# Performance work log

Measured on AMD Instinct MI355X. Metric: run time of the kernel, lower is better.

The kernel has to match this reference:

```python
import jax, jax.numpy as jnp
import numpy as np

B = 4096; NA = 32; DIU = 128; DOU = 32; DIB = 256; DOB = 64; DH = 128; N = NA + 1


def setup_inputs() -> dict:
    key = jax.random.key(0)
    ks = jax.random.split(key, 40)
    kidx = [0]
    def rn(shape, scale=0.1):
        k = ks[kidx[0]]; kidx[0] += 1
        return jax.random.normal(k, shape, jnp.float32) * scale
    inp = {}
    inp['s'] = rn((B, DIU * NA + DIB), 1.0)
    inp['a'] = rn((B, DOU * NA + DOB), 1.0)
    for pre, din in (('ue', DIU + DOU), ('bs', DIB + DOB)):
        inp[pre + '_l1_w'] = rn((din, DH))
        inp[pre + '_l1_b'] = jnp.zeros((DH,), jnp.float32)
        inp[pre + '_l2_w'] = rn((DH, DH))
        inp[pre + '_l2_b'] = jnp.zeros((DH,), jnp.float32)
        for l in range(2):
            inp[pre + f'_gru_wih{l}'] = rn((3 * DH, DH))
            inp[pre + f'_gru_whh{l}'] = rn((3 * DH, DH))
            inp[pre + f'_gru_bih{l}'] = jnp.zeros((3 * DH,), jnp.float32)
            inp[pre + f'_gru_bhh{l}'] = jnp.zeros((3 * DH,), jnp.float32)
    inp['gat_w'] = rn((DH, DH))
    inp['gat_a'] = rn((2 * DH, 1))
    adj = np.zeros((N, N), np.float32)
    adj[1:, 0] = 1.0
    adj[0, 1:] = 1.0  # star graph, as in generate_adjacent_matrix
    inp['adj'] = jnp.asarray(adj)
    inp['ev1_w'] = rn((DH, DH))
    inp['ev1_b'] = jnp.zeros((DH,), jnp.float32)
    inp['ev2_w'] = rn((DH, 1))
    inp['ev2_b'] = jnp.zeros((1,), jnp.float32)
    return inp


def _gru_layer(x, wih, whh, bih, bhh):
    # x: [B, T, H]; torch GRU gate order (r, z, n), weights [3H, H]
    h0 = jnp.zeros((x.shape[0], whh.shape[1]), x.dtype)
    def step(h, xt):
        gi = xt @ wih.T + bih
        gh = h @ whh.T + bhh
        ir, iz, inn = jnp.split(gi, 3, axis=-1)
        hr, hz, hn = jnp.split(gh, 3, axis=-1)
        r = jax.nn.sigmoid(ir + hr)
        z = jax.nn.sigmoid(iz + hz)
        n = jnp.tanh(inn + r * hn)
        h_new = (1.0 - z) * n + z * h
        return h_new, h_new
    _, ys = jax.lax.scan(step, h0, jnp.swapaxes(x, 0, 1))
    return jnp.swapaxes(ys, 0, 1)


def _critic(si, ai, l1w, l1b, l2w, l2b, g0, g1):
    x = jax.nn.relu(jnp.concatenate([si, ai], axis=-1) @ l1w + l1b)
    x = jax.nn.sigmoid(x @ l2w + l2b)
    x = _gru_layer(x, *g0)
    x = _gru_layer(x, *g1)
    return x


def reference(s, a,
              ue_l1_w, ue_l1_b, ue_l2_w, ue_l2_b,
              ue_gru_wih0, ue_gru_whh0, ue_gru_bih0, ue_gru_bhh0,
              ue_gru_wih1, ue_gru_whh1, ue_gru_bih1, ue_gru_bhh1,
              bs_l1_w, bs_l1_b, bs_l2_w, bs_l2_b,
              bs_gru_wih0, bs_gru_whh0, bs_gru_bih0, bs_gru_bhh0,
              bs_gru_wih1, bs_gru_whh1, bs_gru_bih1, bs_gru_bhh1,
              gat_w, gat_a, adj, ev1_w, ev1_b, ev2_w, ev2_b):
    batch = s.shape[0]
    s_ue = s[:, :DIU * NA].reshape(batch, NA, DIU)
    s_bs = s[:, DIU * NA:].reshape(batch, 1, DIB)
    a_ue = a[:, :DOU * NA].reshape(batch, NA, DOU)
    a_bs = a[:, -DOB:].reshape(batch, 1, DOB)
    emb_ue = _critic(s_ue, a_ue, ue_l1_w, ue_l1_b, ue_l2_w, ue_l2_b,
                     (ue_gru_wih0, ue_gru_whh0, ue_gru_bih0, ue_gru_bhh0),
                     (ue_gru_wih1, ue_gru_whh1, ue_gru_bih1, ue_gru_bhh1))
    emb_bs = _critic(s_bs, a_bs, bs_l1_w, bs_l1_b, bs_l2_w, bs_l2_b,
                     (bs_gru_wih0, bs_gru_whh0, bs_gru_bih0, bs_gru_bhh0),
                     (bs_gru_wih1, bs_gru_whh1, bs_gru_bih1, bs_gru_bhh1))
    emb = jnp.concatenate([emb_ue, emb_bs], axis=1)  # [B, N, DH]
    # GAT layer
    Wh = emb @ gat_w                                  # [B, N, DH]
    Wh1 = Wh @ gat_a[:DH]                             # [B, N, 1]
    Wh2 = Wh @ gat_a[DH:]                             # [B, N, 1]
    e = jax.nn.leaky_relu(Wh1 + jnp.swapaxes(Wh2, 1, 2), negative_slope=0.01)
    att = jnp.where(adj > 0, e, jnp.float32(-9e15))
    att = jax.nn.softmax(att, axis=1)                 # NOTE: dim=1, as in source
    # dropout is identity in eval mode
    h_prime = jnp.einsum('bij,bjf->bf', att, Wh)      # matmul + sum over dim 1
    h_prime = jax.nn.elu(h_prime)
    x = jax.nn.relu(h_prime @ ev1_w + ev1_b)
    return x @ ev2_w + ev2_b                          # [B, 1]
```

## Files before the change

kernel.cpp:

```cpp
#include <hip/hip_runtime.h>


typedef unsigned short u16;
typedef __bf16  bf16x8  __attribute__((ext_vector_type(8)));
typedef short   short8  __attribute__((ext_vector_type(8)));
typedef u16     u16x4   __attribute__((ext_vector_type(4)));
typedef float   floatx4 __attribute__((ext_vector_type(4)));

#define DEVI __device__ __forceinline__
#define MFMA(a, b, c) __builtin_amdgcn_mfma_f32_16x16x32_bf16((a), (b), (c), 0, 0, 0)

DEVI u16 f2b(float f) {
    unsigned u = __float_as_uint(f);
    u += 0x7fffu + ((u >> 16) & 1u);
    return (u16)(u >> 16);
}
DEVI float b2f(u16 s) { return __uint_as_float(((unsigned)s) << 16); }
DEVI float sigm(float x) { return 1.f / (1.f + __expf(-x)); }
DEVI float tanh_(float x) { return 1.f - 2.f / (__expf(2.f * x) + 1.f); }

DEVI bf16x8 ldfrag(const u16* q) {
    return *reinterpret_cast<const bf16x8*>(q);
}
DEVI bf16x8 ldfrag_f32(const float* q) {
    float4 u = *reinterpret_cast<const float4*>(q);
    float4 v = *reinterpret_cast<const float4*>(q + 4);
    short8 pk;
    pk[0] = (short)f2b(u.x); pk[1] = (short)f2b(u.y);
    pk[2] = (short)f2b(u.z); pk[3] = (short)f2b(u.w);
    pk[4] = (short)f2b(v.x); pk[5] = (short)f2b(v.y);
    pk[6] = (short)f2b(v.z); pk[7] = (short)f2b(v.w);
    return __builtin_bit_cast(bf16x8, pk);
}

enum : int {
    O_UE_W1T  = 0,
    O_UE_W2T  = 20480,
    O_UE_WIH0 = 36864,
    O_UE_WHH0 = 86016,
    O_UE_WIH1 = 135168,
    O_UE_WHH1 = 184320,
    O_BS_W1T  = 233472,
    O_BS_W2T  = 274432,
    O_BS_WIH0 = 290816,
    O_BS_WIH1 = 339968,
    O_GATWT   = 389120,
    O_EV1T    = 405504,
};
#define WB_X2   1048576u
#define WB_Y0   34603008u
#define WB_SSUM 139460608u

__global__ __launch_bounds__(256) void k_prep(
    const float* __restrict__ ue1, const float* __restrict__ ue2,
    const float* __restrict__ uw0, const float* __restrict__ uh0,
    const float* __restrict__ uw1, const float* __restrict__ uh1,
    const float* __restrict__ bs1, const float* __restrict__ bs2,
    const float* __restrict__ bw0, const float* __restrict__ bw1,
    const float* __restrict__ gw,  const float* __restrict__ e1,
    u16* __restrict__ out)
{
    const int tid = blockIdx.x * blockDim.x + threadIdx.x;
    const int stride = gridDim.x * blockDim.x;
    auto cvt = [&](const float* s, int off, int n) {
        for (int i = tid; i < n; i += stride) out[off + i] = f2b(s[i]);
    };
    auto tcv = [&](const float* s, int off, int K, int N) {
        const int tot = K * N;
        for (int i = tid; i < tot; i += stride) {
            int nn = i / K, kk = i - nn * K;
            out[off + i] = f2b(s[kk * N + nn]);
        }
    };
    tcv(ue1, O_UE_W1T, 160, 128);  tcv(ue2, O_UE_W2T, 128, 128);
    cvt(uw0, O_UE_WIH0, 49152);    cvt(uh0, O_UE_WHH0, 49152);
    cvt(uw1, O_UE_WIH1, 49152);    cvt(uh1, O_UE_WHH1, 49152);
    tcv(bs1, O_BS_W1T, 320, 128);  tcv(bs2, O_BS_W2T, 128, 128);
    cvt(bw0, O_BS_WIH0, 49152);    cvt(bw1, O_BS_WIH1, 49152);
    tcv(gw,  O_GATWT, 128, 128);   tcv(e1,  O_EV1T, 128, 128);
}

__global__ __launch_bounds__(512, 2) void k_ue_l1l2(
    const float* __restrict__ s, const float* __restrict__ a,
    const u16* __restrict__ W1T, const float* __restrict__ b1,
    const u16* __restrict__ W2T, const float* __restrict__ b2,
    u16* __restrict__ X2)
{
    __shared__ __align__(16) u16 A1[128][168];
    __shared__ __align__(16) u16 H[128][136];
    const int tid = threadIdx.x;
    const int w = tid >> 6, lane = tid & 63;
    const int lm = lane & 15, lg = lane >> 4;
    const int r0 = blockIdx.x * 128;

    bf16x8 bw1[5], bw2[4];
#pragma unroll
    for (int ks = 0; ks < 5; ++ks)
        bw1[ks] = ldfrag(W1T + (w * 16 + lm) * 160 + ks * 32 + lg * 8);
#pragma unroll
    for (int ks = 0; ks < 4; ++ks)
        bw2[ks] = ldfrag(W2T + (w * 16 + lm) * 128 + ks * 32 + lg * 8);
    const float bias1 = b1[w * 16 + lm];
    const float bias2 = b2[w * 16 + lm];

#pragma unroll
    for (int it = 0; it < 8; ++it) {
        const int fidx = it * 512 + tid;
        const int row = fidx >> 5, c4 = fidx & 31;
        const int r = r0 + row, bb = r >> 5, tt = r & 31;
        float4 v = *reinterpret_cast<const float4*>(s + (size_t)bb * 4352 + tt * 128 + c4 * 4);
        u16x4 p = {f2b(v.x), f2b(v.y), f2b(v.z), f2b(v.w)};
        *reinterpret_cast<u16x4*>(&A1[row][c4 * 4]) = p;
    }
#pragma unroll
    for (int it = 0; it < 2; ++it) {
        const int fidx = it * 512 + tid;
        const int row = fidx >> 3, c4 = fidx & 7;
        const int r = r0 + row, bb = r >> 5, tt = r & 31;
        float4 v = *reinterpret_cast<const float4*>(a + (size_t)bb * 1088 + tt * 32 + c4 * 4);
        u16x4 p = {f2b(v.x), f2b(v.y), f2b(v.z), f2b(v.w)};
        *reinterpret_cast<u16x4*>(&A1[row][128 + c4 * 4]) = p;
    }
    __syncthreads();

#pragma unroll
    for (int mt = 0; mt < 8; ++mt) {
        bf16x8 af[5];
#pragma unroll
        for (int ks = 0; ks < 5; ++ks)
            af[ks] = ldfrag(&A1[mt * 16 + lm][ks * 32 + lg * 8]);
        floatx4 acc = {0.f, 0.f, 0.f, 0.f};
#pragma unroll
        for (int ks = 0; ks < 5; ++ks) acc = MFMA(af[ks], bw1[ks], acc);
#pragma unroll
        for (int i = 0; i < 4; ++i) {
            float x = acc[i] + bias1;
            H[mt * 16 + lg * 4 + i][w * 16 + lm] = f2b(x > 0.f ? x : 0.f);
        }
    }
    __syncthreads();

#pragma unroll
    for (int mt = 0; mt < 8; ++mt) {
        bf16x8 af[4];
#pragma unroll
        for (int ks = 0; ks < 4; ++ks)
            af[ks] = ldfrag(&H[mt * 16 + lm][ks * 32 + lg * 8]);
        floatx4 acc = {0.f, 0.f, 0.f, 0.f};
#pragma unroll
        for (int ks = 0; ks < 4; ++ks) acc = MFMA(af[ks], bw2[ks], acc);
#pragma unroll
        for (int i = 0; i < 4; ++i)
            X2[(size_t)(r0 + mt * 16 + lg * 4 + i) * 128 + w * 16 + lm] =
                f2b(sigm(acc[i] + bias2));
    }
}

#define SCAN_STEP(RBUF, WBUF, XA, TCUR, PREF_T)                               \
  {                                                                           \
    bf16x8 af[4];                                                             \
    _Pragma("unroll") for (int ks = 0; ks < 4; ++ks)                          \
        af[ks] = ldfrag(&RBUF[lm][ks * 32 + lg * 8]);                         \
    floatx4 accR{0.f,0.f,0.f,0.f}, accZ{0.f,0.f,0.f,0.f};                     \
    floatx4 accGN{0.f,0.f,0.f,0.f}, accHN{0.f,0.f,0.f,0.f};                   \
    __builtin_amdgcn_s_setprio(1);                                            \
    _Pragma("unroll") for (int ks = 0; ks < 4; ++ks) {                        \
        accR  = MFMA(XA[ks], bwi[0][ks], accR);                               \
        accZ  = MFMA(XA[ks], bwi[1][ks], accZ);                               \
        accGN = MFMA(XA[ks], bwi[2][ks], accGN);                              \
    }                                                                         \
    if ((PREF_T) < 32) {                                                      \
        _Pragma("unroll") for (int ks = 0; ks < 4; ++ks)                      \
            XA[ks] = ldfrag(xp + (PREF_T) * 128 + ks * 32);                   \
    }                                                                         \
    _Pragma("unroll") for (int ks = 0; ks < 4; ++ks) {                        \
        accR = MFMA(af[ks], bwh[0][ks], accR);                                \
        accZ = MFMA(af[ks], bwh[1][ks], accZ);                                \
        accHN = MFMA(af[ks], bwh[2][ks], accHN);                              \
    }                                                                         \
    __builtin_amdgcn_s_setprio(0);                                            \
    _Pragma("unroll") for (int i = 0; i < 4; ++i) {                           \
        const float rr = sigm(accR[i] + br);                                  \
        const float zz = sigm(accZ[i] + bz);                                  \
        const float nn = tanh_(accGN[i] + bni + rr * (accHN[i] + bnh));       \
        const float hn = (1.f - zz) * nn + zz * hreg[i];                      \
        hreg[i] = hn;                                                         \
        if (MODE == 1) ssum[i] += hn;                                         \
        const u16 hv = f2b(hn);                                               \
        WBUF[lg * 4 + i][c] = hv;                                             \
        if (MODE == 0)                                                        \
            Y[((size_t)(b0 + lg * 4 + i) * 32 + (TCUR)) * 128 + c] = hv;      \
    }                                                                         \
    __builtin_amdgcn_sched_barrier(0);                                        \
    asm volatile("s_waitcnt lgkmcnt(0)" ::: "memory");                        \
    __builtin_amdgcn_s_barrier();                                             \
    __builtin_amdgcn_sched_barrier(0);                                        \
  }

template <int MODE>
__global__ __launch_bounds__(512, 2) void k_scan(
    const u16* __restrict__ X, const u16* __restrict__ WIH,
    const u16* __restrict__ WHH,
    const float* __restrict__ bih, const float* __restrict__ bhh,
    u16* __restrict__ Y, float* __restrict__ Ssum)
{
    __shared__ __align__(16) u16 hb0[16][136];
    __shared__ __align__(16) u16 hb1[16][136];
    const int w = threadIdx.x >> 6, lane = threadIdx.x & 63;
    const int lm = lane & 15, lg = lane >> 4;
    const int b0 = blockIdx.x * 16;
    const int c = w * 16 + lm;

    bf16x8 bwh[3][4], bwi[3][4];
#pragma unroll
    for (int g = 0; g < 3; ++g)
#pragma unroll
        for (int ks = 0; ks < 4; ++ks) {
            bwh[g][ks] = ldfrag(WHH + (g * 128 + c) * 128 + ks * 32 + lg * 8);
            bwi[g][ks] = ldfrag(WIH + (g * 128 + c) * 128 + ks * 32 + lg * 8);
        }

    for (int i = threadIdx.x; i < 16 * 136; i += 512) {
        ((u16*)hb0)[i] = 0; ((u16*)hb1)[i] = 0;
    }

    const float br  = bih[c] + bhh[c];
    const float bz  = bih[128 + c] + bhh[128 + c];
    const float bni = bih[256 + c], bnh = bhh[256 + c];

    const u16* xp = X + (size_t)(b0 + lm) * 32 * 128 + lg * 8;
    bf16x8 xa[4], xb[4];
#pragma unroll
    for (int ks = 0; ks < 4; ++ks) {
        xa[ks] = ldfrag(xp + ks * 32);
        xb[ks] = ldfrag(xp + 128 + ks * 32);
    }

    float hreg[4] = {}, ssum[4] = {};
    __syncthreads();

    for (int tt = 0; tt < 32; tt += 2) {
        SCAN_STEP(hb0, hb1, xa, tt,     tt + 2);
        SCAN_STEP(hb1, hb0, xb, tt + 1, tt + 3);
    }
    if (MODE == 1) {
#pragma unroll
        for (int i = 0; i < 4; ++i)
            Ssum[(size_t)(b0 + lg * 4 + i) * 128 + c] = ssum[i];
    }
}

__global__ __launch_bounds__(256, 2) void k_bs_final(
    const float* __restrict__ s, const float* __restrict__ a,
    const u16* __restrict__ W1T, const float* __restrict__ b1,
    const u16* __restrict__ W2T, const float* __restrict__ b2,
    const u16* __restrict__ WIH0, const float* __restrict__ bih0,
    const float* __restrict__ bhh0,
    const u16* __restrict__ WIH1, const float* __restrict__ bih1,
    const float* __restrict__ bhh1,
    const float* __restrict__ Ssum,
    const u16* __restrict__ GATWT, const u16* __restrict__ EV1T,
    const float* __restrict__ ev1b, const float* __restrict__ ev2w,
    const float* __restrict__ ev2b, float* __restrict__ out)
{
    __shared__ __align__(16) char smem[52224];
    u16   (*X2L)[136] = reinterpret_cast<u16(*)[136]>(smem);
    u16   (*HBP)[136] = reinterpret_cast<u16(*)[136]>(smem + 17408);
    u16   (*H0L)[136] = reinterpret_cast<u16(*)[136]>(smem + 34816);
    float (*HL)[132]  = reinterpret_cast<float(*)[132]>(smem);
    u16   (*HBF)[136] = reinterpret_cast<u16(*)[136]>(smem + 34816);
    float (*XBF)[132] = reinterpret_cast<float(*)[132]>(smem);

    const int w = threadIdx.x >> 6, lane = threadIdx.x & 63;
    const int lm = lane & 15, lg = lane >> 4;
    const int r0 = blockIdx.x * 64 + w * 16;
    const int lr = w * 16;

    {
        const float* srow = s + (size_t)(r0 + lm) * 4352 + 4096 + lg * 8;
        const float* arow = a + (size_t)(r0 + lm) * 1088 + 1024 + lg * 8;
        bf16x8 af[10];
#pragma unroll
        for (int ks = 0; ks < 8; ++ks) af[ks] = ldfrag_f32(srow + ks * 32);
        af[8] = ldfrag_f32(arow);
        af[9] = ldfrag_f32(arow + 32);

        const u16* wb1 = W1T + lm * 320 + lg * 8;
#pragma unroll
        for (int n = 0; n < 8; ++n) {
            floatx4 acc = {0.f, 0.f, 0.f, 0.f};
#pragma unroll
            for (int ks = 0; ks < 10; ++ks)
                acc = MFMA(af[ks], ldfrag(wb1 + n * 5120 + ks * 32), acc);
            const float bias = b1[n * 16 + lm];
#pragma unroll
            for (int i = 0; i < 4; ++i) {
                float x = acc[i] + bias;
                HBP[lr + lg * 4 + i][n * 16 + lm] = f2b(x > 0.f ? x : 0.f);
            }
        }
        __syncthreads();

        bf16x8 af2[4];
#pragma unroll
        for (int ks = 0; ks < 4; ++ks)
            af2[ks] = ldfrag(&HBP[lr + lm][ks * 32 + lg * 8]);
        const u16* wb2 = W2T + lm * 128 + lg * 8;
#pragma unroll
        for (int n = 0; n < 8; ++n) {
            floatx4 acc = {0.f, 0.f, 0.f, 0.f};
#pragma unroll
            for (int ks = 0; ks < 4; ++ks)
                acc = MFMA(af2[ks], ldfrag(wb2 + n * 2048 + ks * 32), acc);
            const float bias = b2[n * 16 + lm];
#pragma unroll
            for (int i = 0; i < 4; ++i)
                X2L[lr + lg * 4 + i][n * 16 + lm] = f2b(sigm(acc[i] + bias));
        }
    }
    __syncthreads();

    {
        bf16x8 ax[4];
#pragma unroll
        for (int ks = 0; ks < 4; ++ks)
            ax[ks] = ldfrag(&X2L[lr + lm][ks * 32 + lg * 8]);
        floatx4 acc[24];
#pragma unroll
        for (int j = 0; j < 24; ++j) acc[j] = floatx4{0.f, 0.f, 0.f, 0.f};
        const u16* wbp = WIH0 + lm * 128 + lg * 8;
#pragma unroll
        for (int j = 0; j < 24; ++j)
#pragma unroll
            for (int ks = 0; ks < 4; ++ks)
                acc[j] = MFMA(ax[ks], ldfrag(wbp + j * 2048 + ks * 32), acc[j]);
#pragma unroll
        for (int ct = 0; ct < 8; ++ct) {
            const int cc = ct * 16 + lm;
            const float brr = bih0[cc] + bhh0[cc];
            const float bzz = bih0[128 + cc] + bhh0[128 + cc];
            const float bni = bih0[256 + cc], bnh = bhh0[256 + cc];
#pragma unroll
            for (int i = 0; i < 4; ++i) {
                const float rr = sigm(acc[ct][i] + brr);
                const float zz = sigm(acc[8 + ct][i] + bzz);
                const float nn = tanh_(acc[16 + ct][i] + bni + rr * bnh);
                H0L[lr + lg * 4 + i][cc] = f2b((1.f - zz) * nn);
            }
        }
    }
    __syncthreads();

    {
        bf16x8 ax[4];
#pragma unroll
        for (int ks = 0; ks < 4; ++ks)
            ax[ks] = ldfrag(&H0L[lr + lm][ks * 32 + lg * 8]);
        floatx4 acc[24];
#pragma unroll
        for (int j = 0; j < 24; ++j) acc[j] = floatx4{0.f, 0.f, 0.f, 0.f};
        const u16* wbp = WIH1 + lm * 128 + lg * 8;
#pragma unroll
        for (int j = 0; j < 24; ++j)
#pragma unroll
            for (int ks = 0; ks < 4; ++ks)
                acc[j] = MFMA(ax[ks], ldfrag(wbp + j * 2048 + ks * 32), acc[j]);
        __syncthreads();
#pragma unroll
        for (int ct = 0; ct < 8; ++ct) {
            const int cc = ct * 16 + lm;
            const float brr = bih1[cc] + bhh1[cc];
            const float bzz = bih1[128 + cc] + bhh1[128 + cc];
            const float bni = bih1[256 + cc], bnh = bhh1[256 + cc];
#pragma unroll
            for (int i = 0; i < 4; ++i) {
                const float rr = sigm(acc[ct][i] + brr);
                const float zz = sigm(acc[8 + ct][i] + bzz);
                const float nn = tanh_(acc[16 + ct][i] + bni + rr * bnh);
                HL[lr + lg * 4 + i][cc] = (1.f - zz) * nn;
            }
        }
    }
    __syncthreads();

    {
        const float* p1 = Ssum + (size_t)(r0 + lm) * 128 + lg * 8;
        bf16x8 af[4];
#pragma unroll
        for (int ks = 0; ks < 4; ++ks) {
            float4 u  = *reinterpret_cast<const float4*>(p1 + ks * 32);
            float4 u2 = *reinterpret_cast<const float4*>(p1 + ks * 32 + 4);
            float4 v  = *reinterpret_cast<const float4*>(&HL[lr + lm][ks * 32 + lg * 8]);
            float4 v2 = *reinterpret_cast<const float4*>(&HL[lr + lm][ks * 32 + lg * 8 + 4]);
            short8 pk;
            pk[0] = (short)f2b(u.x + v.x);  pk[1] = (short)f2b(u.y + v.y);
            pk[2] = (short)f2b(u.z + v.z);  pk[3] = (short)f2b(u.w + v.w);
            pk[4] = (short)f2b(u2.x + v2.x); pk[5] = (short)f2b(u2.y + v2.y);
            pk[6] = (short)f2b(u2.z + v2.z); pk[7] = (short)f2b(u2.w + v2.w);
            af[ks] = __builtin_bit_cast(bf16x8, pk);
        }
        __syncthreads();
        const u16* gwp = GATWT + lm * 128 + lg * 8;
#pragma unroll
        for (int n = 0; n < 8; ++n) {
            floatx4 acc = {0.f, 0.f, 0.f, 0.f};
#pragma unroll
            for (int ks = 0; ks < 4; ++ks)
                acc = MFMA(af[ks], ldfrag(gwp + n * 2048 + ks * 32), acc);
#pragma unroll
            for (int i = 0; i < 4; ++i) {
                float x = acc[i];
                x = x > 0.f ? x : (__expf(x) - 1.f);
                HBF[lr + lg * 4 + i][n * 16 + lm] = f2b(x);
            }
        }
        __syncthreads();

        bf16x8 af2[4];
#pragma unroll
        for (int ks = 0; ks < 4; ++ks)
            af2[ks] = ldfrag(&HBF[lr + lm][ks * 32 + lg * 8]);
        const u16* e1p = EV1T + lm * 128 + lg * 8;
#pragma unroll
        for (int n = 0; n < 8; ++n) {
            floatx4 acc = {0.f, 0.f, 0.f, 0.f};
#pragma unroll
            for (int ks = 0; ks < 4; ++ks)
                acc = MFMA(af2[ks], ldfrag(e1p + n * 2048 + ks * 32), acc);
            const float bias = ev1b[n * 16 + lm];
#pragma unroll
            for (int i = 0; i < 4; ++i) {
                float v = acc[i] + bias;
                XBF[lr + lg * 4 + i][n * 16 + lm] = v > 0.f ? v : 0.f;
            }
        }
        __syncthreads();

        float sacc = 0.f;
#pragma unroll
        for (int k = 0; k < 32; ++k) {
            const int cc = lg * 32 + k;
            sacc += XBF[lr + lm][cc] * ev2w[cc];
        }
        sacc += __shfl_xor(sacc, 16, 64);
        sacc += __shfl_xor(sacc, 32, 64);
        if (lg == 0) out[r0 + lm] = sacc + ev2b[0];
    }
}

extern "C" void kernel_launch(void* const* d_in, const int* in_sizes, int n_in,
                              void* d_out, int out_size, void* d_ws, size_t ws_size,
                              hipStream_t stream)
{
    (void)in_sizes; (void)n_in; (void)out_size; (void)ws_size;
    const float* s       = (const float*)d_in[0];
    const float* a       = (const float*)d_in[1];
    const float* ue_l1_w = (const float*)d_in[2];
    const float* ue_l1_b = (const float*)d_in[3];
    const float* ue_l2_w = (const float*)d_in[4];
    const float* ue_l2_b = (const float*)d_in[5];
    const float* ue_wih0 = (const float*)d_in[6];
    const float* ue_whh0 = (const float*)d_in[7];
    const float* ue_bih0 = (const float*)d_in[8];
    const float* ue_bhh0 = (const float*)d_in[9];
    const float* ue_wih1 = (const float*)d_in[10];
    const float* ue_whh1 = (const float*)d_in[11];
    const float* ue_bih1 = (const float*)d_in[12];
    const float* ue_bhh1 = (const float*)d_in[13];
    const float* bs_l1_w = (const float*)d_in[14];
    const float* bs_l1_b = (const float*)d_in[15];
    const float* bs_l2_w = (const float*)d_in[16];
    const float* bs_l2_b = (const float*)d_in[17];
    const float* bs_wih0 = (const float*)d_in[18];
    const float* bs_bih0 = (const float*)d_in[20];
    const float* bs_bhh0 = (const float*)d_in[21];
    const float* bs_wih1 = (const float*)d_in[22];
    const float* bs_bih1 = (const float*)d_in[24];
    const float* bs_bhh1 = (const float*)d_in[25];
    const float* gat_w   = (const float*)d_in[26];
    const float* ev1_w   = (const float*)d_in[29];
    const float* ev1_b   = (const float*)d_in[30];
    const float* ev2_w   = (const float*)d_in[31];
    const float* ev2_b   = (const float*)d_in[32];

    char* ws = (char*)d_ws;
    u16*   wb   = (u16*)ws;
    u16*   X2   = (u16*)(ws + WB_X2);
    u16*   Y0   = (u16*)(ws + WB_Y0);
    float* SSUM = (float*)(ws + WB_SSUM);

    k_prep<<<256, 256, 0, stream>>>(ue_l1_w, ue_l2_w, ue_wih0, ue_whh0,
                                    ue_wih1, ue_whh1, bs_l1_w, bs_l2_w,
                                    bs_wih0, bs_wih1, gat_w, ev1_w, wb);
    k_ue_l1l2<<<1024, 512, 0, stream>>>(s, a, wb + O_UE_W1T, ue_l1_b,
                                        wb + O_UE_W2T, ue_l2_b, X2);
    k_scan<0><<<256, 512, 0, stream>>>(X2, wb + O_UE_WIH0, wb + O_UE_WHH0,
                                       ue_bih0, ue_bhh0, Y0, nullptr);
    k_scan<1><<<256, 512, 0, stream>>>(Y0, wb + O_UE_WIH1, wb + O_UE_WHH1,
                                       ue_bih1, ue_bhh1, nullptr, SSUM);
    k_bs_final<<<64, 256, 0, stream>>>(s, a, wb + O_BS_W1T, bs_l1_b,
                                       wb + O_BS_W2T, bs_l2_b,
                                       wb + O_BS_WIH0, bs_bih0, bs_bhh0,
                                       wb + O_BS_WIH1, bs_bih1, bs_bhh1,
                                       SSUM, wb + O_GATWT, wb + O_EV1T,
                                       ev1_b, ev2_w, ev2_b, (float*)d_out);
}
```

Before: 359.3 us.

## Repartition final BS kernel so each wave owns output columns, not rows

Restructures k_bs_final from 64 blocks of 4 waves, each wave computing all 128 output columns for its own 16 rows, to 256 blocks of 8 waves that share 16 rows, with each wave computing one 16-column slice. Every layer now exchanges activations through shared memory with a barrier between layers. The aim is to spread the BS critic tail across more CUs and cut per-wave serial MFMA chains and accumulator register pressure. The cost is more barriers and more weight-fragment loads per block, since each block rereads all weights for only 16 rows.

```diff
diff --git a/kernel.cpp b/kernel.cpp
--- a/kernel.cpp
+++ b/kernel.cpp
@@ -250,7 +250,7 @@
     }
 }
 
-__global__ __launch_bounds__(256, 2) void k_bs_final(
+__global__ __launch_bounds__(512, 1) void k_bs_final(
     const float* __restrict__ s, const float* __restrict__ a,
     const u16* __restrict__ W1T, const float* __restrict__ b1,
     const u16* __restrict__ W2T, const float* __restrict__ b2,
@@ -263,18 +263,17 @@
     const float* __restrict__ ev1b, const float* __restrict__ ev2w,
     const float* __restrict__ ev2b, float* __restrict__ out)
 {
-    __shared__ __align__(16) char smem[52224];
-    u16   (*X2L)[136] = reinterpret_cast<u16(*)[136]>(smem);
-    u16   (*HBP)[136] = reinterpret_cast<u16(*)[136]>(smem + 17408);
-    u16   (*H0L)[136] = reinterpret_cast<u16(*)[136]>(smem + 34816);
-    float (*HL)[132]  = reinterpret_cast<float(*)[132]>(smem);
-    u16   (*HBF)[136] = reinterpret_cast<u16(*)[136]>(smem + 34816);
-    float (*XBF)[132] = reinterpret_cast<float(*)[132]>(smem);
+    __shared__ __align__(16) u16 HBl[16][136];
+    __shared__ __align__(16) u16 X2b[16][136];
+    __shared__ __align__(16) u16 H0b[16][136];
+    __shared__ __align__(16) float HLf[16][132];
+    __shared__ __align__(16) u16 HBe[16][136];
+    __shared__ __align__(16) float XBf[16][132];
 
     const int w = threadIdx.x >> 6, lane = threadIdx.x & 63;
     const int lm = lane & 15, lg = lane >> 4;
-    const int r0 = blockIdx.x * 64 + w * 16;
-    const int lr = w * 16;
+    const int r0 = blockIdx.x * 16;
+    const int c = w * 16 + lm;
 
     {
         const float* srow = s + (size_t)(r0 + lm) * 4352 + 4096 + lg * 8;
@@ -285,166 +284,161 @@
         af[8] = ldfrag_f32(arow);
         af[9] = ldfrag_f32(arow + 32);
 
-        const u16* wb1 = W1T + lm * 320 + lg * 8;
-#pragma unroll
-        for (int n = 0; n < 8; ++n) {
-            floatx4 acc = {0.f, 0.f, 0.f, 0.f};
-#pragma unroll
-            for (int ks = 0; ks < 10; ++ks)
-                acc = MFMA(af[ks], ldfrag(wb1 + n * 5120 + ks * 32), acc);
-            const float bias = b1[n * 16 + lm];
-#pragma unroll
-            for (int i = 0; i < 4; ++i) {
-                float x = acc[i] + bias;
-                HBP[lr + lg * 4 + i][n * 16 + lm] = f2b(x > 0.f ? x : 0.f);
-            }
-        }
-        __syncthreads();
-
-        bf16x8 af2[4];
-#pragma unroll
-        for (int ks = 0; ks < 4; ++ks)
-            af2[ks] = ldfrag(&HBP[lr + lm][ks * 32 + lg * 8]);
-        const u16* wb2 = W2T + lm * 128 + lg * 8;
-#pragma unroll
-        for (int n = 0; n < 8; ++n) {
-            floatx4 acc = {0.f, 0.f, 0.f, 0.f};
-#pragma unroll
-            for (int ks = 0; ks < 4; ++ks)
-                acc = MFMA(af2[ks], ldfrag(wb2 + n * 2048 + ks * 32), acc);
-            const float bias = b2[n * 16 + lm];
-#pragma unroll
-            for (int i = 0; i < 4; ++i)
-                X2L[lr + lg * 4 + i][n * 16 + lm] = f2b(sigm(acc[i] + bias));
-        }
-    }
-    __syncthreads();
-
-    {
-        bf16x8 ax[4];
-#pragma unroll
-        for (int ks = 0; ks < 4; ++ks)
-            ax[ks] = ldfrag(&X2L[lr + lm][ks * 32 + lg * 8]);
-        floatx4 acc[24];
-#pragma unroll
-        for (int j = 0; j < 24; ++j) acc[j] = floatx4{0.f, 0.f, 0.f, 0.f};
-        const u16* wbp = WIH0 + lm * 128 + lg * 8;
-#pragma unroll
-        for (int j = 0; j < 24; ++j)
-#pragma unroll
-            for (int ks = 0; ks < 4; ++ks)
-                acc[j] = MFMA(ax[ks], ldfrag(wbp + j * 2048 + ks * 32), acc[j]);
-#pragma unroll
-        for (int ct = 0; ct < 8; ++ct) {
-            const int cc = ct * 16 + lm;
-            const float brr = bih0[cc] + bhh0[cc];
-            const float bzz = bih0[128 + cc] + bhh0[128 + cc];
-            const float bni = bih0[256 + cc], bnh = bhh0[256 + cc];
-#pragma unroll
-            for (int i = 0; i < 4; ++i) {
-                const float rr = sigm(acc[ct][i] + brr);
-                const float zz = sigm(acc[8 + ct][i] + bzz);
-                const float nn = tanh_(acc[16 + ct][i] + bni + rr * bnh);
-                H0L[lr + lg * 4 + i][cc] = f2b((1.f - zz) * nn);
-            }
-        }
-    }
-    __syncthreads();
-
-    {
-        bf16x8 ax[4];
-#pragma unroll
-        for (int ks = 0; ks < 4; ++ks)
-            ax[ks] = ldfrag(&H0L[lr + lm][ks * 32 + lg * 8]);
-        floatx4 acc[24];
-#pragma unroll
-        for (int j = 0; j < 24; ++j) acc[j] = floatx4{0.f, 0.f, 0.f, 0.f};
-        const u16* wbp = WIH1 + lm * 128 + lg * 8;
-#pragma unroll
-        for (int j = 0; j < 24; ++j)
-#pragma unroll
-            for (int ks = 0; ks < 4; ++ks)
-                acc[j] = MFMA(ax[ks], ldfrag(wbp + j * 2048 + ks * 32), acc[j]);
-        __syncthreads();
-#pragma unroll
-        for (int ct = 0; ct < 8; ++ct) {
-            const int cc = ct * 16 + lm;
-            const float brr = bih1[cc] + bhh1[cc];
-            const float bzz = bih1[128 + cc] + bhh1[128 + cc];
-            const float bni = bih1[256 + cc], bnh = bhh1[256 + cc];
-#pragma unroll
-            for (int i = 0; i < 4; ++i) {
-                const float rr = sigm(acc[ct][i] + brr);
-                const float zz = sigm(acc[8 + ct][i] + bzz);
-                const float nn = tanh_(acc[16 + ct][i] + bni + rr * bnh);
-                HL[lr + lg * 4 + i][cc] = (1.f - zz) * nn;
-            }
-        }
-    }
-    __syncthreads();
-
+        bf16x8 bw[10];
+#pragma unroll
+        for (int ks = 0; ks < 10; ++ks)
+            bw[ks] = ldfrag(W1T + c * 320 + ks * 32 + lg * 8);
+        floatx4 acc = {0.f, 0.f, 0.f, 0.f};
+#pragma unroll
+        for (int ks = 0; ks < 10; ++ks) acc = MFMA(af[ks], bw[ks], acc);
+        const float bias = b1[c];
+#pragma unroll
+        for (int i = 0; i < 4; ++i) {
+            float x = acc[i] + bias;
+            HBl[lg * 4 + i][c] = f2b(x > 0.f ? x : 0.f);
+        }
+    }
+    __syncthreads();
+
+    {
+        bf16x8 af[4], bw[4];
+#pragma unroll
+        for (int ks = 0; ks < 4; ++ks) {
+            af[ks] = ldfrag(&HBl[lm][ks * 32 + lg * 8]);
+            bw[ks] = ldfrag(W2T + c * 128 + ks * 32 + lg * 8);
+        }
+        floatx4 acc = {0.f, 0.f, 0.f, 0.f};
+#pragma unroll
+        for (int ks = 0; ks < 4; ++ks) acc = MFMA(af[ks], bw[ks], acc);
+        const float bias = b2[c];
+#pragma unroll
+        for (int i = 0; i < 4; ++i)
+            X2b[lg * 4 + i][c] = f2b(sigm(acc[i] + bias));
+    }
+    __syncthreads();
+
+    {
+        bf16x8 af[4], bw[3][4];
+#pragma unroll
+        for (int ks = 0; ks < 4; ++ks) {
+            af[ks] = ldfrag(&X2b[lm][ks * 32 + lg * 8]);
+#pragma unroll
+            for (int g = 0; g < 3; ++g)
+                bw[g][ks] = ldfrag(WIH0 + (g * 128 + c) * 128 + ks * 32 + lg * 8);
+        }
+        floatx4 aR{0,0,0,0}, aZ{0,0,0,0}, aN{0,0,0,0};
+#pragma unroll
+        for (int ks = 0; ks < 4; ++ks) {
+            aR = MFMA(af[ks], bw[0][ks], aR);
+            aZ = MFMA(af[ks], bw[1][ks], aZ);
+            aN = MFMA(af[ks], bw[2][ks], aN);
+        }
+        const float brr = bih0[c] + bhh0[c];
+        const float bzz = bih0[128 + c] + bhh0[128 + c];
+        const float bni = bih0[256 + c], bnh = bhh0[256 + c];
+#pragma unroll
+        for (int i = 0; i < 4; ++i) {
+            const float rr = sigm(aR[i] + brr);
+            const float zz = sigm(aZ[i] + bzz);
+            const float nn = tanh_(aN[i] + bni + rr * bnh);
+            H0b[lg * 4 + i][c] = f2b((1.f - zz) * nn);
+        }
+    }
+    __syncthreads();
+
+    float4 ssA[4], ssB[4];
     {
         const float* p1 = Ssum + (size_t)(r0 + lm) * 128 + lg * 8;
-        bf16x8 af[4];
-#pragma unroll
-        for (int ks = 0; ks < 4; ++ks) {
-            float4 u  = *reinterpret_cast<const float4*>(p1 + ks * 32);
-            float4 u2 = *reinterpret_cast<const float4*>(p1 + ks * 32 + 4);
-            float4 v  = *reinterpret_cast<const float4*>(&HL[lr + lm][ks * 32 + lg * 8]);
-            float4 v2 = *reinterpret_cast<const float4*>(&HL[lr + lm][ks * 32 + lg * 8 + 4]);
+#pragma unroll
+        for (int ks = 0; ks < 4; ++ks) {
+            ssA[ks] = *reinterpret_cast<const float4*>(p1 + ks * 32);
+            ssB[ks] = *reinterpret_cast<const float4*>(p1 + ks * 32 + 4);
+        }
+        bf16x8 af[4], bw[3][4];
+#pragma unroll
+        for (int ks = 0; ks < 4; ++ks) {
+            af[ks] = ldfrag(&H0b[lm][ks * 32 + lg * 8]);
+#pragma unroll
+            for (int g = 0; g < 3; ++g)
+                bw[g][ks] = ldfrag(WIH1 + (g * 128 + c) * 128 + ks * 32 + lg * 8);
+        }
+        floatx4 aR{0,0,0,0}, aZ{0,0,0,0}, aN{0,0,0,0};
+#pragma unroll
+        for (int ks = 0; ks < 4; ++ks) {
+            aR = MFMA(af[ks], bw[0][ks], aR);
+            aZ = MFMA(af[ks], bw[1][ks], aZ);
+            aN = MFMA(af[ks], bw[2][ks], aN);
+        }
+        const float brr = bih1[c] + bhh1[c];
+        const float bzz = bih1[128 + c] + bhh1[128 + c];
+        const float bni = bih1[256 + c], bnh = bhh1[256 + c];
+#pragma unroll
+        for (int i = 0; i < 4; ++i) {
+            const float rr = sigm(aR[i] + brr);
+            const float zz = sigm(aZ[i] + bzz);
+            const float nn = tanh_(aN[i] + bni + rr * bnh);
+            HLf[lg * 4 + i][c] = (1.f - zz) * nn;
+        }
+    }
+    __syncthreads();
+
+    {
+        bf16x8 af[4], bw[4];
+#pragma unroll
+        for (int ks = 0; ks < 4; ++ks) {
+            const float* hl = &HLf[lm][ks * 32 + lg * 8];
+            float4 v  = *reinterpret_cast<const float4*>(hl);
+            float4 v2 = *reinterpret_cast<const float4*>(hl + 4);
             short8 pk;
-            pk[0] = (short)f2b(u.x + v.x);  pk[1] = (short)f2b(u.y + v.y);
-            pk[2] = (short)f2b(u.z + v.z);  pk[3] = (short)f2b(u.w + v.w);
-            pk[4] = (short)f2b(u2.x + v2.x); pk[5] = (short)f2b(u2.y + v2.y);
-            pk[6] = (short)f2b(u2.z + v2.z); pk[7] = (short)f2b(u2.w + v2.w);
+            pk[0] = (short)f2b(ssA[ks].x + v.x);  pk[1] = (short)f2b(ssA[ks].y + v.y);
+            pk[2] = (short)f2b(ssA[ks].z + v.z);  pk[3] = (short)f2b(ssA[ks].w + v.w);
+            pk[4] = (short)f2b(ssB[ks].x + v2.x); pk[5] = (short)f2b(ssB[ks].y + v2.y);
+            pk[6] = (short)f2b(ssB[ks].z + v2.z); pk[7] = (short)f2b(ssB[ks].w + v2.w);
             af[ks] = __builtin_bit_cast(bf16x8, pk);
-        }
-        __syncthreads();
-        const u16* gwp = GATWT + lm * 128 + lg * 8;
-#pragma unroll
-        for (int n = 0; n < 8; ++n) {
-            floatx4 acc = {0.f, 0.f, 0.f, 0.f};
-#pragma unroll
-            for (int ks = 0; ks < 4; ++ks)
-                acc = MFMA(af[ks], ldfrag(gwp + n * 2048 + ks * 32), acc);
-#pragma unroll
-            for (int i = 0; i < 4; ++i) {
-                float x = acc[i];
-                x = x > 0.f ? x : (__expf(x) - 1.f);
-                HBF[lr + lg * 4 + i][n * 16 + lm] = f2b(x);
-            }
-        }
-        __syncthreads();
-
-        bf16x8 af2[4];
-#pragma unroll
-        for (int ks = 0; ks < 4; ++ks)
-            af2[ks] = ldfrag(&HBF[lr + lm][ks * 32 + lg * 8]);
-        const u16* e1p = EV1T + lm * 128 + lg * 8;
-#pragma unroll
-        for (int n = 0; n < 8; ++n) {
-            floatx4 acc = {0.f, 0.f, 0.f, 0.f};
-#pragma unroll
-            for (int ks = 0; ks < 4; ++ks)
-                acc = MFMA(af2[ks], ldfrag(e1p + n * 2048 + ks * 32), acc);
-            const float bias = ev1b[n * 16 + lm];
-#pragma unroll
-            for (int i = 0; i < 4; ++i) {
-                float v = acc[i] + bias;
-                XBF[lr + lg * 4 + i][n * 16 + lm] = v > 0.f ? v : 0.f;
-            }
-        }
-        __syncthreads();
-
+            bw[ks] = ldfrag(GATWT + c * 128 + ks * 32 + lg * 8);
+        }
+        floatx4 acc = {0.f, 0.f, 0.f, 0.f};
+#pragma unroll
+        for (int ks = 0; ks < 4; ++ks) acc = MFMA(af[ks], bw[ks], acc);
+#pragma unroll
+        for (int i = 0; i < 4; ++i) {
+            float x = acc[i];
+            x = x > 0.f ? x : (__expf(x) - 1.f);
+            HBe[lg * 4 + i][c] = f2b(x);
+        }
+    }
+    __syncthreads();
+
+    {
+        bf16x8 af[4], bw[4];
+#pragma unroll
+        for (int ks = 0; ks < 4; ++ks) {
+            af[ks] = ldfrag(&HBe[lm][ks * 32 + lg * 8]);
+            bw[ks] = ldfrag(EV1T + c * 128 + ks * 32 + lg * 8);
+        }
+        floatx4 acc = {0.f, 0.f, 0.f, 0.f};
+#pragma unroll
+        for (int ks = 0; ks < 4; ++ks) acc = MFMA(af[ks], bw[ks], acc);
+        const float bias = ev1b[c];
+#pragma unroll
+        for (int i = 0; i < 4; ++i) {
+            float v = acc[i] + bias;
+            XBf[lg * 4 + i][c] = v > 0.f ? v : 0.f;
+        }
+    }
+    __syncthreads();
+
+    {
+        const int row = threadIdx.x >> 5, l5 = threadIdx.x & 31;
         float sacc = 0.f;
 #pragma unroll
-        for (int k = 0; k < 32; ++k) {
-            const int cc = lg * 32 + k;
-            sacc += XBF[lr + lm][cc] * ev2w[cc];
-        }
-        sacc += __shfl_xor(sacc, 16, 64);
-        sacc += __shfl_xor(sacc, 32, 64);
-        if (lg == 0) out[r0 + lm] = sacc + ev2b[0];
+        for (int j = 0; j < 4; ++j) {
+            const int cc = l5 * 4 + j;
+            sacc += XBf[row][cc] * ev2w[cc];
+        }
+#pragma unroll
+        for (int d = 1; d < 32; d <<= 1) sacc += __shfl_xor(sacc, d, 64);
+        if (l5 == 0) out[r0 + row] = sacc + ev2b[0];
     }
 }
 
@@ -498,10 +492,10 @@
                                        ue_bih0, ue_bhh0, Y0, nullptr);
     k_scan<1><<<256, 512, 0, stream>>>(Y0, wb + O_UE_WIH1, wb + O_UE_WHH1,
                                        ue_bih1, ue_bhh1, nullptr, SSUM);
-    k_bs_final<<<64, 256, 0, stream>>>(s, a, wb + O_BS_W1T, bs_l1_b,
-                                       wb + O_BS_W2T, bs_l2_b,
-                                       wb + O_BS_WIH0, bs_bih0, bs_bhh0,
-                                       wb + O_BS_WIH1, bs_bih1, bs_bhh1,
-                                       SSUM, wb + O_GATWT, wb + O_EV1T,
-                                       ev1_b, ev2_w, ev2_b, (float*)d_out);
-}
+    k_bs_final<<<256, 512, 0, stream>>>(s, a, wb + O_BS_W1T, bs_l1_b,
+                                        wb + O_BS_W2T, bs_l2_b,
+                                        wb + O_BS_WIH0, bs_bih0, bs_bhh0,
+                                        wb + O_BS_WIH1, bs_bih1, bs_bhh1,
+                                        SSUM, wb + O_GATWT, wb + O_EV1T,
+                                        ev1_b, ev2_w, ev2_b, (float*)d_out);
+}
```

After: 306.9 us. 1.17x faster.
